# Performance work log

Measured on AMD Instinct MI355X. Metric: run time of the kernel, lower is better.

## Reference

```python
import jax, jax.numpy as jnp
import numpy as np
from jax import lax

# Model dims (mamba_ssm defaults: d_state=16, d_conv=4, expand=2, dt_rank=ceil(d_model/16))
V = 16384       # vocab_size
D = 1024        # embedding_dim / d_model
C_CLS = 128     # num_CLS_classes
D_INNER = 2 * D # expand * d_model = 2048
N = 16          # d_state
K = 4           # d_conv
DT_RANK = (D + 15) // 16  # 64
B, L = 4, 512


def setup_inputs() -> dict:
    key = jax.random.key(0)
    ks = jax.random.split(key, 12)
    s = 0.02
    tokens = jax.random.randint(ks[0], (B, L), 0, V, dtype=jnp.int64)
    embedding = jax.random.normal(ks[1], (V, D), jnp.float32) * s
    in_proj_w = jax.random.normal(ks[2], (2 * D_INNER, D), jnp.float32) * s
    conv_w = jax.random.normal(ks[3], (D_INNER, 1, K), jnp.float32) * 0.1
    conv_b = jnp.zeros((D_INNER,), jnp.float32)
    x_proj_w = jax.random.normal(ks[4], (DT_RANK + 2 * N, D_INNER), jnp.float32) * s
    dt_proj_w = jax.random.normal(ks[5], (D_INNER, DT_RANK), jnp.float32) * s
    dt_proj_b = jax.random.uniform(ks[6], (D_INNER,), jnp.float32, -4.0, -2.0)  # softplus -> small dt
    A_log = jnp.log(jnp.broadcast_to(jnp.arange(1, N + 1, dtype=jnp.float32), (D_INNER, N)))
    D_param = jnp.ones((D_INNER,), jnp.float32)
    out_proj_w = jax.random.normal(ks[7], (D, D_INNER), jnp.float32) * s
    recon_w = jax.random.normal(ks[8], (V, D), jnp.float32) * s
    cls_w = jax.random.normal(ks[9], (C_CLS, D), jnp.float32) * s
    return dict(tokens=tokens, embedding=embedding, in_proj_w=in_proj_w,
                conv_w=conv_w, conv_b=conv_b, x_proj_w=x_proj_w,
                dt_proj_w=dt_proj_w, dt_proj_b=dt_proj_b, A_log=A_log,
                D_param=D_param, out_proj_w=out_proj_w, recon_w=recon_w, cls_w=cls_w)


def _mamba(h, in_proj_w, conv_w, conv_b, x_proj_w, dt_proj_w, dt_proj_b, A_log, D_param, out_proj_w):
    # h: (B, L, D)
    xz = jnp.einsum('bld,ed->ble', h, in_proj_w)          # (B, L, 2*D_INNER)
    x, z = jnp.split(xz, 2, axis=-1)                      # each (B, L, D_INNER)
    # causal depthwise conv1d along L
    xt = jnp.swapaxes(x, 1, 2)                            # (B, D_INNER, L)
    xt = lax.conv_general_dilated(xt, conv_w, window_strides=(1,),
                                  padding=[(K - 1, 0)],
                                  feature_group_count=D_INNER,
                                  dimension_numbers=('NCH', 'OIH', 'NCH'))
    xt = xt + conv_b[None, :, None]
    x = jax.nn.silu(jnp.swapaxes(xt, 1, 2))               # (B, L, D_INNER)
    # input-dependent dt, B, C
    x_dbl = jnp.einsum('bld,ed->ble', x, x_proj_w)        # (B, L, DT_RANK+2N)
    dt, Bm, Cm = jnp.split(x_dbl, [DT_RANK, DT_RANK + N], axis=-1)
    delta = jax.nn.softplus(jnp.einsum('blr,dr->bld', dt, dt_proj_w) + dt_proj_b)  # (B,L,D_INNER)
    A = -jnp.exp(A_log)                                   # (D_INNER, N)
    dA = jnp.exp(delta[..., None] * A)                    # (B,L,D_INNER,N)
    dBx = delta[..., None] * Bm[:, :, None, :] * x[..., None]  # (B,L,D_INNER,N)
    # selective scan over time (sequential recurrence)
    dA_t = jnp.swapaxes(dA, 0, 1)                         # (L,B,D_INNER,N)
    dBx_t = jnp.swapaxes(dBx, 0, 1)
    C_t = jnp.swapaxes(Cm, 0, 1)                          # (L,B,N)
    def step(hc, inp):
        a, bx, c = inp
        hc = a * hc + bx                                  # (B,D_INNER,N)
        y = jnp.einsum('bdn,bn->bd', hc, c)
        return hc, y
    h0 = jnp.zeros((x.shape[0], D_INNER, N), x.dtype)
    _, ys = lax.scan(step, h0, (dA_t, dBx_t, C_t))
    y = jnp.swapaxes(ys, 0, 1) + x * D_param              # (B,L,D_INNER)
    y = y * jax.nn.silu(z)
    return jnp.einsum('ble,de->bld', y, out_proj_w)       # (B,L,D)


def reference(tokens, embedding, in_proj_w, conv_w, conv_b, x_proj_w,
              dt_proj_w, dt_proj_b, A_log, D_param, out_proj_w, recon_w, cls_w):
    h = embedding[tokens]                                 # (B,L,D)
    h = _mamba(h, in_proj_w, conv_w, conv_b, x_proj_w, dt_proj_w, dt_proj_b,
               A_log, D_param, out_proj_w)
    recon = jnp.einsum('bld,vd->blv', h, recon_w)         # (B,L,V)
    pooled = h.mean(axis=1)                               # mean CLS pooling assumption
    cls = jnp.einsum('bd,cd->bc', pooled, cls_w)          # (B,C_CLS)
    return (recon, cls)
```

## Files before the change

kernel.cpp:

```cpp
#include <hip/hip_runtime.h>
#include <hip/hip_bf16.h>
#include <stdint.h>

#define DIN    2048
#define MROWS  2048
#define LSEQ   512
#define NV     16384
#define DMODEL 1024
#define NC     8
#define CL     64

typedef __attribute__((ext_vector_type(8))) short bf16x8;
typedef __attribute__((ext_vector_type(4))) float f32x4;

__device__ __forceinline__ uint16_t f2bf(float f) {
  uint32_t u = __builtin_bit_cast(uint32_t, f);
  u += 0x7fffu + ((u >> 16) & 1u);
  return (uint16_t)(u >> 16);
}
__device__ __forceinline__ float bf2f(uint16_t u) {
  return __builtin_bit_cast(float, (uint32_t)u << 16);
}

__device__ __forceinline__ void gld_lds16(const uint16_t* g, uint16_t* l) {
  __builtin_amdgcn_global_load_lds(
      (const __attribute__((address_space(1))) void*)g,
      (__attribute__((address_space(3))) void*)l,
      16, 0, 0);
}

__global__ __launch_bounds__(512, 2) void gemm256_bf16_kernel(
    const uint16_t* __restrict__ A, const uint16_t* __restrict__ B,
    float* __restrict__ C, int M, int N, int K)
{
  __shared__ uint16_t lds[4 * 16384];
  const int tid = threadIdx.x;
  const int w   = tid >> 6;
  const int l   = tid & 63;

  const int nwg = gridDim.x;
  const int cpx = nwg >> 3;
  const int swz = (blockIdx.x & 7) * cpx + (blockIdx.x >> 3);
  const int nmy = M >> 8;
  const int bm  = (swz % nmy) << 8;
  const int bn  = (swz / nmy) << 8;

  const int fr = l & 15;
  const int fg = l >> 4;
  const int wr = w >> 2;
  const int wc = w & 3;

  const int srow = l >> 2;
  const int kof  = (((l & 3) ^ ((l >> 3) & 3)) << 3);
  const int ar0  = (w * 2 + 0) * 16 + srow;
  const int ar1  = (w * 2 + 1) * 16 + srow;
  const uint16_t* Ag0 = A + (size_t)(bm + ar0) * K + kof;
  const uint16_t* Ag1 = A + (size_t)(bm + ar1) * K + kof;
  const uint16_t* Bg0 = B + (size_t)(bn + ar0) * K + kof;
  const uint16_t* Bg1 = B + (size_t)(bn + ar1) * K + kof;
  const int lA0 = (w * 2 + 0) * 512;
  const int lA1 = (w * 2 + 1) * 512;
  const int lB0 = 8192 + (w * 2 + 0) * 512;
  const int lB1 = 8192 + (w * 2 + 1) * 512;

  const int axr  = ((fg ^ ((fr >> 1) & 3)) << 3);
  const int aoff = (wr * 128 + fr) * 32 + axr;
  const int boff = 8192 + (wc * 64 + fr) * 32 + axr;

  f32x4 acc[8][4] = {};
  const int NT = K >> 5;

  auto stage = [&](int t) {
    const int sb = (t & 3) << 14;
    const int k0 = t << 5;
    gld_lds16(Ag0 + k0, lds + sb + lA0);
    gld_lds16(Ag1 + k0, lds + sb + lA1);
    gld_lds16(Bg0 + k0, lds + sb + lB0);
    gld_lds16(Bg1 + k0, lds + sb + lB1);
  };
  auto compute_tile = [&](int sb) {
    bf16x8 af[8], bfr[4];
#pragma unroll
    for (int mi = 0; mi < 8; ++mi)
      af[mi] = *(const bf16x8*)(lds + sb + aoff + mi * 512);
#pragma unroll
    for (int ni = 0; ni < 4; ++ni)
      bfr[ni] = *(const bf16x8*)(lds + sb + boff + ni * 512);
    __builtin_amdgcn_s_setprio(1);
#pragma unroll
    for (int mi = 0; mi < 8; ++mi)
#pragma unroll
      for (int ni = 0; ni < 4; ++ni)
        acc[mi][ni] = __builtin_amdgcn_mfma_f32_16x16x32_bf16(af[mi], bfr[ni], acc[mi][ni], 0, 0, 0);
    __builtin_amdgcn_s_setprio(0);
  };

  stage(0); stage(1); stage(2);
  asm volatile("s_waitcnt vmcnt(8)" ::: "memory");
  __builtin_amdgcn_s_barrier();

  for (int t = 0; t < NT - 3; ++t) {
    stage(t + 3);
    compute_tile((t & 3) << 14);
    asm volatile("s_waitcnt vmcnt(8)" ::: "memory");
    __builtin_amdgcn_s_barrier();
  }
  compute_tile(((NT - 3) & 3) << 14);
  asm volatile("s_waitcnt vmcnt(4)" ::: "memory");
  __builtin_amdgcn_s_barrier();
  compute_tile(((NT - 2) & 3) << 14);
  asm volatile("s_waitcnt vmcnt(0)" ::: "memory");
  __builtin_amdgcn_s_barrier();
  compute_tile(((NT - 1) & 3) << 14);

#pragma unroll
  for (int mi = 0; mi < 8; ++mi) {
    const int r0 = bm + wr * 128 + mi * 16 + fg * 4;
#pragma unroll
    for (int ni = 0; ni < 4; ++ni) {
      const int c0 = bn + wc * 64 + ni * 16 + fr;
#pragma unroll
      for (int r = 0; r < 4; ++r)
        C[(size_t)(r0 + r) * N + c0] = acc[mi][ni][r];
    }
  }
}

__global__ __launch_bounds__(256) void gemm_bf16_kernel(
    const uint16_t* __restrict__ A, const uint16_t* __restrict__ B,
    float* __restrict__ Cf, uint16_t* __restrict__ Cbf,
    int M, int N, int K, int kchunk, const float* __restrict__ bias)
{
  __shared__ uint16_t As[128 * 32];
  __shared__ uint16_t Bs[128 * 32];
  const int tid  = threadIdx.x;
  const int wid  = tid >> 6;
  const int lane = tid & 63;
  const int bm = blockIdx.y * 128;
  const int bn = blockIdx.x * 128;
  const int k_beg = blockIdx.z * kchunk;
  float* Cout = Cf + (size_t)blockIdx.z * M * N;

  const int fr = lane & 15;
  const int fg = lane >> 4;
  const int wm = (wid >> 1) * 64;
  const int wn = (wid & 1) * 64;

  const int srow = wid * 32 + (lane >> 2);
  const int skof = (((lane & 3) ^ ((lane >> 2) & 3)) << 3);
  const uint16_t* Ag = A + (size_t)(bm + srow) * K + skof;
  const uint16_t* Bg = B + (size_t)(bn + srow) * K + skof;
  uint16_t* Al = As + wid * 1024;
  uint16_t* Bl = Bs + wid * 1024;

  const int cxr = ((fg ^ (fr & 3)) << 3);

  f32x4 acc[4][4] = {};

  for (int k0 = 0; k0 < kchunk; k0 += 32) {
    const int kk = k_beg + k0;
    gld_lds16(Ag + kk, Al);
    gld_lds16(Ag + (size_t)16 * K + kk, Al + 512);
    gld_lds16(Bg + kk, Bl);
    gld_lds16(Bg + (size_t)16 * K + kk, Bl + 512);
    asm volatile("s_waitcnt vmcnt(0)" ::: "memory");
    __syncthreads();
    bf16x8 af[4], bfr[4];
#pragma unroll
    for (int i = 0; i < 4; ++i)
      af[i] = *(const bf16x8*)(As + (wm + i * 16 + fr) * 32 + cxr);
#pragma unroll
    for (int j = 0; j < 4; ++j)
      bfr[j] = *(const bf16x8*)(Bs + (wn + j * 16 + fr) * 32 + cxr);
#pragma unroll
    for (int i = 0; i < 4; ++i)
#pragma unroll
      for (int j = 0; j < 4; ++j)
        acc[i][j] = __builtin_amdgcn_mfma_f32_16x16x32_bf16(af[i], bfr[j], acc[i][j], 0, 0, 0);
    __syncthreads();
  }

#pragma unroll
  for (int i = 0; i < 4; ++i) {
    const int r0 = bm + wm + i * 16 + fg * 4;
#pragma unroll
    for (int j = 0; j < 4; ++j) {
      const int c0 = bn + wn + j * 16 + fr;
      const float bv = bias ? bias[c0] : 0.f;
#pragma unroll
      for (int r = 0; r < 4; ++r) {
        float v = acc[i][j][r];
        if (bias) {
          const float u = v + bv;
          v = (u > 20.f) ? u : log1pf(__expf(u));
        }
        if (Cbf) Cbf[(size_t)(r0 + r) * N + c0] = f2bf(v);
        else     Cout[(size_t)(r0 + r) * N + c0] = v;
      }
    }
  }
}

__global__ __launch_bounds__(256) void cvt_weights_kernel(
    const float* __restrict__ wo, const float* __restrict__ wdt, const float* __restrict__ wx,
    uint16_t* __restrict__ wob, uint16_t* __restrict__ wdtb, uint16_t* __restrict__ wxb)
{
  const int bid = blockIdx.x;
  if (bid < 2048) {
    const int i = bid * 256 + threadIdx.x;
    const float4 v = ((const float4*)wo)[i];
    ((ushort4*)wob)[i] = make_ushort4(f2bf(v.x), f2bf(v.y), f2bf(v.z), f2bf(v.w));
  } else if (bid < 2176) {
    const int i = (bid - 2048) * 256 + threadIdx.x;
    const float4 v = ((const float4*)wdt)[i];
    ((ushort4*)wdtb)[i] = make_ushort4(f2bf(v.x), f2bf(v.y), f2bf(v.z), f2bf(v.w));
  } else {
    const int i = (bid - 2176) * 256 + threadIdx.x;
    const int r = i >> 9, c = i & 511;
    ushort4 o = make_ushort4(0, 0, 0, 0);
    if (r < 96) {
      const float4 v = ((const float4*)wx)[(size_t)r * 512 + c];
      o = make_ushort4(f2bf(v.x), f2bf(v.y), f2bf(v.z), f2bf(v.w));
    }
    ((ushort4*)wxb)[i] = o;
  }
}

__global__ __launch_bounds__(256) void reduce8_dt_kernel(
    const float* __restrict__ in, float* __restrict__ xdbl, uint16_t* __restrict__ dtb) {
  const int i = blockIdx.x * 256 + threadIdx.x;
  float s = 0.f;
#pragma unroll
  for (int z = 0; z < 8; ++z) s += in[i + (size_t)z * 262144];
  xdbl[i] = s;
  const int c = i & 127;
  if (c < 64) dtb[(i >> 7) * 64 + c] = f2bf(s);
}

__global__ __launch_bounds__(256) void reduce2_bf16_kernel(
    const float* __restrict__ in, uint16_t* __restrict__ outb, int n) {
  const int i = blockIdx.x * 256 + threadIdx.x;
  if (i >= n) return;
  outb[i] = f2bf(in[i] + in[i + (size_t)n]);
}

__global__ __launch_bounds__(256) void embed_kernel(
    const int* __restrict__ tok, const float* __restrict__ emb, uint16_t* __restrict__ out) {
  const int m = blockIdx.x;
  const int t = tok[m];
  const float4 v = ((const float4*)(emb + (size_t)t * DMODEL))[threadIdx.x];
  ((ushort4*)(out + (size_t)m * DMODEL))[threadIdx.x] =
      make_ushort4(f2bf(v.x), f2bf(v.y), f2bf(v.z), f2bf(v.w));
}

__global__ __launch_bounds__(256) void cvt_bf16_kernel(
    const float* __restrict__ in, uint16_t* __restrict__ out, int n4) {
  const int i = blockIdx.x * 256 + threadIdx.x;
  if (i >= n4) return;
  const float4 v = ((const float4*)in)[i];
  ((ushort4*)out)[i] = make_ushort4(f2bf(v.x), f2bf(v.y), f2bf(v.z), f2bf(v.w));
}

__global__ __launch_bounds__(256) void conv_silu_kernel(
    const uint16_t* __restrict__ xzb, const float* __restrict__ cw, const float* __restrict__ cb,
    uint16_t* __restrict__ xcb)
{
  const int idx = blockIdx.x * 256 + threadIdx.x;
  const int d4  = idx & 511;
  const int m   = idx >> 9;
  const int l   = m & (LSEQ - 1);
  const int d   = d4 << 2;
  const float4 cbv = *(const float4*)(cb + d);
  float a0 = cbv.x, a1 = cbv.y, a2 = cbv.z, a3 = cbv.w;
  const float4 w0 = *(const float4*)(cw + (d + 0) * 4);
  const float4 w1 = *(const float4*)(cw + (d + 1) * 4);
  const float4 w2 = *(const float4*)(cw + (d + 2) * 4);
  const float4 w3 = *(const float4*)(cw + (d + 3) * 4);
  const float wj0[4] = {w0.x, w0.y, w0.z, w0.w};
  const float wj1[4] = {w1.x, w1.y, w1.z, w1.w};
  const float wj2[4] = {w2.x, w2.y, w2.z, w2.w};
  const float wj3[4] = {w3.x, w3.y, w3.z, w3.w};
#pragma unroll
  for (int j = 0; j < 4; ++j) {
    const int lj = l - 3 + j;
    if (lj >= 0) {
      const ushort4 x = *(const ushort4*)(xzb + (size_t)(m - 3 + j) * 4096 + d);
      a0 += wj0[j] * bf2f(x.x);
      a1 += wj1[j] * bf2f(x.y);
      a2 += wj2[j] * bf2f(x.z);
      a3 += wj3[j] * bf2f(x.w);
    }
  }
  const float r0 = a0 / (1.f + __expf(-a0));
  const float r1 = a1 / (1.f + __expf(-a1));
  const float r2 = a2 / (1.f + __expf(-a2));
  const float r3 = a3 / (1.f + __expf(-a3));
  *(ushort4*)(xcb + (size_t)m * DIN + d) = make_ushort4(f2bf(r0), f2bf(r1), f2bf(r2), f2bf(r3));
}

__global__ __launch_bounds__(256) void scan_partial_kernel(
    const float* __restrict__ delta, const uint16_t* __restrict__ xcb,
    const float* __restrict__ xdbl, const float* __restrict__ A_log,
    float* __restrict__ Pb, float* __restrict__ Qb)
{
  const int q = threadIdx.x & 3;
  const int d_idx = threadIdx.x >> 2;
  const int c = blockIdx.x;
  const int d = blockIdx.y * 64 + d_idx;
  const int b = blockIdx.z;
  float Arow[4];
#pragma unroll
  for (int n = 0; n < 4; ++n)
    Arow[n] = -expf(A_log[d * 16 + q * 4 + n]);
  float P[4] = {1.f, 1.f, 1.f, 1.f};
  float Q[4] = {0.f, 0.f, 0.f, 0.f};
  const int l0 = c * CL;
#pragma unroll 4
  for (int li = 0; li < CL; ++li) {
    const int m = b * LSEQ + l0 + li;
    const float de = delta[(size_t)m * DIN + d];
    const float xv = bf2f(xcb[(size_t)m * DIN + d]);
    const float dx = de * xv;
    const float4 Bv = *(const float4*)(xdbl + (size_t)m * 128 + 64 + q * 4);
    const float bv[4] = {Bv.x, Bv.y, Bv.z, Bv.w};
#pragma unroll
    for (int n = 0; n < 4; ++n) {
      const float a = __expf(de * Arow[n]);
      P[n] *= a;
      Q[n] = a * Q[n] + dx * bv[n];
    }
  }
  const size_t o = ((size_t)(b * NC + c) * DIN + d) * 16 + q * 4;
  *(float4*)(Pb + o) = make_float4(P[0], P[1], P[2], P[3]);
  *(float4*)(Qb + o) = make_float4(Q[0], Q[1], Q[2], Q[3]);
}

__global__ __launch_bounds__(256) void scan_bounds_kernel(
    const float* __restrict__ Pb, const float* __restrict__ Qb, float* __restrict__ Hi)
{
  const int i = blockIdx.x * 256 + threadIdx.x;
  const int b = i >> 15;
  const int r = i & 32767;
  float h = 0.f;
#pragma unroll
  for (int c = 0; c < NC; ++c) {
    const size_t o = ((size_t)(b * NC + c) << 15) + r;
    Hi[o] = h;
    h = Pb[o] * h + Qb[o];
  }
}

__global__ __launch_bounds__(256) void scan_final_kernel(
    const float* __restrict__ delta, const uint16_t* __restrict__ xcb,
    const float* __restrict__ xdbl, const uint16_t* __restrict__ xzb,
    const float* __restrict__ A_log, const float* __restrict__ Dp,
    const float* __restrict__ Hi, uint16_t* __restrict__ yb)
{
  const int q = threadIdx.x & 3;
  const int d_idx = threadIdx.x >> 2;
  const int c = blockIdx.x;
  const int d = blockIdx.y * 64 + d_idx;
  const int b = blockIdx.z;
  float Arow[4];
#pragma unroll
  for (int n = 0; n < 4; ++n)
    Arow[n] = -expf(A_log[d * 16 + q * 4 + n]);
  const float dpd = Dp[d];
  const size_t o = ((size_t)(b * NC + c) * DIN + d) * 16 + q * 4;
  const float4 Hv = *(const float4*)(Hi + o);
  float h[4] = {Hv.x, Hv.y, Hv.z, Hv.w};
  const int l0 = c * CL;
#pragma unroll 2
  for (int li = 0; li < CL; ++li) {
    const int m = b * LSEQ + l0 + li;
    const float de = delta[(size_t)m * DIN + d];
    const float xv = bf2f(xcb[(size_t)m * DIN + d]);
    const float dx = de * xv;
    const float4 Bv = *(const float4*)(xdbl + (size_t)m * 128 + 64 + q * 4);
    const float4 Cv = *(const float4*)(xdbl + (size_t)m * 128 + 80 + q * 4);
    const float bv[4] = {Bv.x, Bv.y, Bv.z, Bv.w};
    const float cv[4] = {Cv.x, Cv.y, Cv.z, Cv.w};
    float yp = 0.f;
#pragma unroll
    for (int n = 0; n < 4; ++n) {
      const float a = __expf(de * Arow[n]);
      h[n] = a * h[n] + dx * bv[n];
      yp += h[n] * cv[n];
    }
    yp += __shfl_xor(yp, 1);
    yp += __shfl_xor(yp, 2);
    if (q == 0) {
      const float z = bf2f(xzb[(size_t)m * 4096 + 2048 + d]);
      const float sil = z / (1.f + __expf(-z));
      yb[(size_t)m * DIN + d] = f2bf((yp + xv * dpd) * sil);
    }
  }
}

__global__ __launch_bounds__(256) void pool1_kernel(
    const uint16_t* __restrict__ h2b, float* __restrict__ part) {
  const int b = blockIdx.x >> 4, s = blockIdx.x & 15;
  const int c = threadIdx.x * 4;
  const uint16_t* base = h2b + ((size_t)(b * LSEQ + s * 32)) * DMODEL + c;
  float a0 = 0, a1 = 0, a2 = 0, a3 = 0;
  for (int l = 0; l < 32; ++l) {
    const ushort4 v = *(const ushort4*)(base + (size_t)l * DMODEL);
    a0 += bf2f(v.x); a1 += bf2f(v.y); a2 += bf2f(v.z); a3 += bf2f(v.w);
  }
  *(float4*)(part + (size_t)blockIdx.x * DMODEL + c) = make_float4(a0, a1, a2, a3);
}

__global__ __launch_bounds__(256) void pool2_cls_kernel(
    const float* __restrict__ part, const float* __restrict__ w, float* __restrict__ out) {
  __shared__ float pl[DMODEL];
  const int b = blockIdx.x, t = threadIdx.x;
  float4 s = make_float4(0, 0, 0, 0);
  for (int k = 0; k < 16; ++k) {
    const float4 v = *(const float4*)(part + ((size_t)(b * 16 + k)) * DMODEL + t * 4);
    s.x += v.x; s.y += v.y; s.z += v.z; s.w += v.w;
  }
  const float inv = 1.f / (float)LSEQ;
  pl[t * 4 + 0] = s.x * inv; pl[t * 4 + 1] = s.y * inv;
  pl[t * 4 + 2] = s.z * inv; pl[t * 4 + 3] = s.w * inv;
  __syncthreads();
  if (t < 128) {
    const float* wr = w + (size_t)t * DMODEL;
    float acc = 0.f;
    for (int k = 0; k < DMODEL; ++k) acc += pl[k] * wr[k];
    out[b * 128 + t] = acc;
  }
}

extern "C" void kernel_launch(void* const* d_in, const int* in_sizes, int n_in,
                              void* d_out, int out_size, void* d_ws, size_t ws_size,
                              hipStream_t stream) {
  const int*   tokens    = (const int*)d_in[0];
  const float* embedding = (const float*)d_in[1];
  const float* in_proj_w = (const float*)d_in[2];
  const float* conv_w    = (const float*)d_in[3];
  const float* conv_b    = (const float*)d_in[4];
  const float* x_proj_w  = (const float*)d_in[5];
  const float* dt_proj_w = (const float*)d_in[6];
  const float* dt_proj_b = (const float*)d_in[7];
  const float* A_log     = (const float*)d_in[8];
  const float* D_param   = (const float*)d_in[9];
  const float* out_prj_w = (const float*)d_in[10];
  const float* recon_w   = (const float*)d_in[11];
  const float* cls_w     = (const float*)d_in[12];

  char* ws = (char*)d_ws;
  const size_t MB = 1024 * 1024;
  uint16_t* h_bf   = (uint16_t*)(ws + 0);
  uint16_t* w_in   = (uint16_t*)(ws + 4 * MB);
  uint16_t* xz_bf  = (uint16_t*)(ws + 12 * MB);
  uint16_t* xc_b   = (uint16_t*)(ws + 28 * MB);
  uint16_t* wx_bf  = (uint16_t*)(ws + 36 * MB);
  uint16_t* dt_bf  = (uint16_t*)(ws + 36 * MB + 512 * 1024);
  uint16_t* wdt_bf = (uint16_t*)(ws + 36 * MB + 768 * 1024);
  float*    xdbl   = (float*)(ws + 37 * MB);
  float*    delta  = (float*)(ws + 38 * MB);
  float*    Pbuf   = (float*)(ws + 54 * MB);
  float*    Qbuf   = (float*)(ws + 58 * MB);
  uint16_t* y_bf   = (uint16_t*)(ws + 62 * MB);
  uint16_t* h2_bf  = (uint16_t*)(ws + 70 * MB);
  float*    part   = (float*)(ws + 74 * MB);
  uint16_t* wout_bf = h_bf;
  float*    Hinit   = (float*)(ws + 4 * MB);
  float*    kscr    = delta;
  uint16_t* wrec_bf = (uint16_t*)(ws + 38 * MB);

  const int RECON = MROWS * NV;

  embed_kernel<<<dim3(MROWS), dim3(256), 0, stream>>>(tokens, embedding, h_bf);
  cvt_bf16_kernel<<<dim3(4096), dim3(256), 0, stream>>>(in_proj_w, w_in, 4096 * 1024 / 4);
  gemm_bf16_kernel<<<dim3(32, 16, 1), dim3(256), 0, stream>>>(h_bf, w_in, nullptr, xz_bf, MROWS, 4096, 1024, 1024, nullptr);
  cvt_weights_kernel<<<dim3(2432), dim3(256), 0, stream>>>(out_prj_w, dt_proj_w, x_proj_w, wout_bf, wdt_bf, wx_bf);
  conv_silu_kernel<<<dim3(4096), dim3(256), 0, stream>>>(xz_bf, conv_w, conv_b, xc_b);
  gemm_bf16_kernel<<<dim3(1, 16, 8), dim3(256), 0, stream>>>(xc_b, wx_bf, kscr, nullptr, MROWS, 128, 2048, 256, nullptr);
  reduce8_dt_kernel<<<dim3(1024), dim3(256), 0, stream>>>(kscr, xdbl, dt_bf);
  gemm_bf16_kernel<<<dim3(16, 16, 1), dim3(256), 0, stream>>>(dt_bf, wdt_bf, delta, nullptr, MROWS, DIN, 64, 64, dt_proj_b);
  scan_partial_kernel<<<dim3(NC, 32, 4), dim3(256), 0, stream>>>(delta, xc_b, xdbl, A_log, Pbuf, Qbuf);
  scan_bounds_kernel<<<dim3(512), dim3(256), 0, stream>>>(Pbuf, Qbuf, Hinit);
  scan_final_kernel<<<dim3(NC, 32, 4), dim3(256), 0, stream>>>(delta, xc_b, xdbl, xz_bf, A_log, D_param, Hinit, y_bf);
  gemm_bf16_kernel<<<dim3(8, 16, 2), dim3(256), 0, stream>>>(y_bf, wout_bf, kscr, nullptr, MROWS, 1024, 2048, 1024, nullptr);
  reduce2_bf16_kernel<<<dim3(8192), dim3(256), 0, stream>>>(kscr, h2_bf, MROWS * 1024);
  cvt_bf16_kernel<<<dim3(16384), dim3(256), 0, stream>>>(recon_w, wrec_bf, NV * 1024 / 4);
  gemm256_bf16_kernel<<<dim3(512), dim3(512), 0, stream>>>(h2_bf, wrec_bf, (float*)d_out, MROWS, NV, 1024);
  pool1_kernel<<<dim3(64), dim3(256), 0, stream>>>(h2_bf, part);
  pool2_cls_kernel<<<dim3(4), dim3(256), 0, stream>>>(part, cls_w, (float*)d_out + RECON);
}
```

Baseline: 359.2 us.

## Fuse scan stages, merge conversion kernels, store delta in bf16, drop split-K

Merges the embedding gather and all weight conversions into one kernel. Fuses the three chunked-scan kernels into one block-level kernel that does the chunk carry in shared memory. Stores delta as bf16 instead of fp32, and runs the out_proj GEMM without split-K so it writes bf16 directly, which removes the reduce2 kernel. This cuts launches and HBM round trips for the P/Q/H buffers and delta. In exchange the out_proj GEMM runs fewer blocks over a longer K, and delta loses precision.

```diff
diff --git a/kernel.cpp b/kernel.cpp
--- a/kernel.cpp
+++ b/kernel.cpp
@@ -201,21 +201,35 @@
   }
 }
 
-__global__ __launch_bounds__(256) void cvt_weights_kernel(
-    const float* __restrict__ wo, const float* __restrict__ wdt, const float* __restrict__ wx,
-    uint16_t* __restrict__ wob, uint16_t* __restrict__ wdtb, uint16_t* __restrict__ wxb)
+__global__ __launch_bounds__(256) void mega_cvt_kernel(
+    const int* __restrict__ tok, const float* __restrict__ emb,
+    const float* __restrict__ wi, const float* __restrict__ wo,
+    const float* __restrict__ wdt, const float* __restrict__ wx,
+    uint16_t* __restrict__ hb, uint16_t* __restrict__ wib,
+    uint16_t* __restrict__ wob, uint16_t* __restrict__ wdtb,
+    uint16_t* __restrict__ wxb)
 {
   const int bid = blockIdx.x;
   if (bid < 2048) {
-    const int i = bid * 256 + threadIdx.x;
+    const int m = bid;
+    const int t = tok[m];
+    const float4 v = ((const float4*)(emb + (size_t)t * DMODEL))[threadIdx.x];
+    ((ushort4*)(hb + (size_t)m * DMODEL))[threadIdx.x] =
+        make_ushort4(f2bf(v.x), f2bf(v.y), f2bf(v.z), f2bf(v.w));
+  } else if (bid < 6144) {
+    const int i = (bid - 2048) * 256 + threadIdx.x;
+    const float4 v = ((const float4*)wi)[i];
+    ((ushort4*)wib)[i] = make_ushort4(f2bf(v.x), f2bf(v.y), f2bf(v.z), f2bf(v.w));
+  } else if (bid < 8192) {
+    const int i = (bid - 6144) * 256 + threadIdx.x;
     const float4 v = ((const float4*)wo)[i];
     ((ushort4*)wob)[i] = make_ushort4(f2bf(v.x), f2bf(v.y), f2bf(v.z), f2bf(v.w));
-  } else if (bid < 2176) {
-    const int i = (bid - 2048) * 256 + threadIdx.x;
+  } else if (bid < 8320) {
+    const int i = (bid - 8192) * 256 + threadIdx.x;
     const float4 v = ((const float4*)wdt)[i];
     ((ushort4*)wdtb)[i] = make_ushort4(f2bf(v.x), f2bf(v.y), f2bf(v.z), f2bf(v.w));
   } else {
-    const int i = (bid - 2176) * 256 + threadIdx.x;
+    const int i = (bid - 8320) * 256 + threadIdx.x;
     const int r = i >> 9, c = i & 511;
     ushort4 o = make_ushort4(0, 0, 0, 0);
     if (r < 96) {
@@ -235,22 +249,6 @@
   xdbl[i] = s;
   const int c = i & 127;
   if (c < 64) dtb[(i >> 7) * 64 + c] = f2bf(s);
-}
-
-__global__ __launch_bounds__(256) void reduce2_bf16_kernel(
-    const float* __restrict__ in, uint16_t* __restrict__ outb, int n) {
-  const int i = blockIdx.x * 256 + threadIdx.x;
-  if (i >= n) return;
-  outb[i] = f2bf(in[i] + in[i + (size_t)n]);
-}
-
-__global__ __launch_bounds__(256) void embed_kernel(
-    const int* __restrict__ tok, const float* __restrict__ emb, uint16_t* __restrict__ out) {
-  const int m = blockIdx.x;
-  const int t = tok[m];
-  const float4 v = ((const float4*)(emb + (size_t)t * DMODEL))[threadIdx.x];
-  ((ushort4*)(out + (size_t)m * DMODEL))[threadIdx.x] =
-      make_ushort4(f2bf(v.x), f2bf(v.y), f2bf(v.z), f2bf(v.w));
 }
 
 __global__ __launch_bounds__(256) void cvt_bf16_kernel(
@@ -298,27 +296,32 @@
   *(ushort4*)(xcb + (size_t)m * DIN + d) = make_ushort4(f2bf(r0), f2bf(r1), f2bf(r2), f2bf(r3));
 }
 
-__global__ __launch_bounds__(256) void scan_partial_kernel(
-    const float* __restrict__ delta, const uint16_t* __restrict__ xcb,
-    const float* __restrict__ xdbl, const float* __restrict__ A_log,
-    float* __restrict__ Pb, float* __restrict__ Qb)
+__global__ __launch_bounds__(256) void scan_fused_kernel(
+    const uint16_t* __restrict__ delta_bf, const uint16_t* __restrict__ xcb,
+    const float* __restrict__ xdbl, const uint16_t* __restrict__ xzb,
+    const float* __restrict__ A_log, const float* __restrict__ Dp,
+    uint16_t* __restrict__ yb)
 {
+  __shared__ float Ps[NC][8][4][4];
+  __shared__ float Qs[NC][8][4][4];
+  __shared__ float Hs[NC][8][4][4];
   const int q = threadIdx.x & 3;
-  const int d_idx = threadIdx.x >> 2;
-  const int c = blockIdx.x;
-  const int d = blockIdx.y * 64 + d_idx;
-  const int b = blockIdx.z;
+  const int d_idx = (threadIdx.x >> 2) & 7;
+  const int c = threadIdx.x >> 5;
+  const int d = blockIdx.x * 8 + d_idx;
+  const int b = blockIdx.y;
   float Arow[4];
 #pragma unroll
   for (int n = 0; n < 4; ++n)
     Arow[n] = -expf(A_log[d * 16 + q * 4 + n]);
+  const int l0 = c * CL;
+
   float P[4] = {1.f, 1.f, 1.f, 1.f};
   float Q[4] = {0.f, 0.f, 0.f, 0.f};
-  const int l0 = c * CL;
 #pragma unroll 4
   for (int li = 0; li < CL; ++li) {
     const int m = b * LSEQ + l0 + li;
-    const float de = delta[(size_t)m * DIN + d];
+    const float de = bf2f(delta_bf[(size_t)m * DIN + d]);
     const float xv = bf2f(xcb[(size_t)m * DIN + d]);
     const float dx = de * xv;
     const float4 Bv = *(const float4*)(xdbl + (size_t)m * 128 + 64 + q * 4);
@@ -330,50 +333,34 @@
       Q[n] = a * Q[n] + dx * bv[n];
     }
   }
-  const size_t o = ((size_t)(b * NC + c) * DIN + d) * 16 + q * 4;
-  *(float4*)(Pb + o) = make_float4(P[0], P[1], P[2], P[3]);
-  *(float4*)(Qb + o) = make_float4(Q[0], Q[1], Q[2], Q[3]);
-}
-
-__global__ __launch_bounds__(256) void scan_bounds_kernel(
-    const float* __restrict__ Pb, const float* __restrict__ Qb, float* __restrict__ Hi)
-{
-  const int i = blockIdx.x * 256 + threadIdx.x;
-  const int b = i >> 15;
-  const int r = i & 32767;
-  float h = 0.f;
-#pragma unroll
-  for (int c = 0; c < NC; ++c) {
-    const size_t o = ((size_t)(b * NC + c) << 15) + r;
-    Hi[o] = h;
-    h = Pb[o] * h + Qb[o];
-  }
-}
-
-__global__ __launch_bounds__(256) void scan_final_kernel(
-    const float* __restrict__ delta, const uint16_t* __restrict__ xcb,
-    const float* __restrict__ xdbl, const uint16_t* __restrict__ xzb,
-    const float* __restrict__ A_log, const float* __restrict__ Dp,
-    const float* __restrict__ Hi, uint16_t* __restrict__ yb)
-{
-  const int q = threadIdx.x & 3;
-  const int d_idx = threadIdx.x >> 2;
-  const int c = blockIdx.x;
-  const int d = blockIdx.y * 64 + d_idx;
-  const int b = blockIdx.z;
-  float Arow[4];
-#pragma unroll
-  for (int n = 0; n < 4; ++n)
-    Arow[n] = -expf(A_log[d * 16 + q * 4 + n]);
+#pragma unroll
+  for (int n = 0; n < 4; ++n) {
+    Ps[c][d_idx][q][n] = P[n];
+    Qs[c][d_idx][q][n] = Q[n];
+  }
+  __syncthreads();
+
+  if (threadIdx.x < 32) {
+    float h[4] = {0.f, 0.f, 0.f, 0.f};
+#pragma unroll
+    for (int cc = 0; cc < NC; ++cc) {
+#pragma unroll
+      for (int n = 0; n < 4; ++n) {
+        Hs[cc][d_idx][q][n] = h[n];
+        h[n] = Ps[cc][d_idx][q][n] * h[n] + Qs[cc][d_idx][q][n];
+      }
+    }
+  }
+  __syncthreads();
+
+  float h[4];
+#pragma unroll
+  for (int n = 0; n < 4; ++n) h[n] = Hs[c][d_idx][q][n];
   const float dpd = Dp[d];
-  const size_t o = ((size_t)(b * NC + c) * DIN + d) * 16 + q * 4;
-  const float4 Hv = *(const float4*)(Hi + o);
-  float h[4] = {Hv.x, Hv.y, Hv.z, Hv.w};
-  const int l0 = c * CL;
 #pragma unroll 2
   for (int li = 0; li < CL; ++li) {
     const int m = b * LSEQ + l0 + li;
-    const float de = delta[(size_t)m * DIN + d];
+    const float de = bf2f(delta_bf[(size_t)m * DIN + d]);
     const float xv = bf2f(xcb[(size_t)m * DIN + d]);
     const float dx = de * xv;
     const float4 Bv = *(const float4*)(xdbl + (size_t)m * 128 + 64 + q * 4);
@@ -458,32 +445,26 @@
   uint16_t* dt_bf  = (uint16_t*)(ws + 36 * MB + 512 * 1024);
   uint16_t* wdt_bf = (uint16_t*)(ws + 36 * MB + 768 * 1024);
   float*    xdbl   = (float*)(ws + 37 * MB);
-  float*    delta  = (float*)(ws + 38 * MB);
-  float*    Pbuf   = (float*)(ws + 54 * MB);
-  float*    Qbuf   = (float*)(ws + 58 * MB);
-  uint16_t* y_bf   = (uint16_t*)(ws + 62 * MB);
-  uint16_t* h2_bf  = (uint16_t*)(ws + 70 * MB);
-  float*    part   = (float*)(ws + 74 * MB);
-  uint16_t* wout_bf = h_bf;
-  float*    Hinit   = (float*)(ws + 4 * MB);
-  float*    kscr    = delta;
-  uint16_t* wrec_bf = (uint16_t*)(ws + 38 * MB);
+  uint16_t* delt_b = (uint16_t*)(ws + 38 * MB);
+  float*    kscr   = (float*)(ws + 46 * MB);
+  uint16_t* y_bf   = (uint16_t*)(ws + 54 * MB);
+  uint16_t* h2_bf  = (uint16_t*)(ws + 62 * MB);
+  uint16_t* wout_bf= (uint16_t*)(ws + 66 * MB);
+  float*    part   = (float*)(ws + 70 * MB);
+  uint16_t* wrec_bf= (uint16_t*)(ws + 71 * MB);
 
   const int RECON = MROWS * NV;
 
-  embed_kernel<<<dim3(MROWS), dim3(256), 0, stream>>>(tokens, embedding, h_bf);
-  cvt_bf16_kernel<<<dim3(4096), dim3(256), 0, stream>>>(in_proj_w, w_in, 4096 * 1024 / 4);
+  mega_cvt_kernel<<<dim3(8576), dim3(256), 0, stream>>>(
+      tokens, embedding, in_proj_w, out_prj_w, dt_proj_w, x_proj_w,
+      h_bf, w_in, wout_bf, wdt_bf, wx_bf);
   gemm_bf16_kernel<<<dim3(32, 16, 1), dim3(256), 0, stream>>>(h_bf, w_in, nullptr, xz_bf, MROWS, 4096, 1024, 1024, nullptr);
-  cvt_weights_kernel<<<dim3(2432), dim3(256), 0, stream>>>(out_prj_w, dt_proj_w, x_proj_w, wout_bf, wdt_bf, wx_bf);
   conv_silu_kernel<<<dim3(4096), dim3(256), 0, stream>>>(xz_bf, conv_w, conv_b, xc_b);
   gemm_bf16_kernel<<<dim3(1, 16, 8), dim3(256), 0, stream>>>(xc_b, wx_bf, kscr, nullptr, MROWS, 128, 2048, 256, nullptr);
   reduce8_dt_kernel<<<dim3(1024), dim3(256), 0, stream>>>(kscr, xdbl, dt_bf);
-  gemm_bf16_kernel<<<dim3(16, 16, 1), dim3(256), 0, stream>>>(dt_bf, wdt_bf, delta, nullptr, MROWS, DIN, 64, 64, dt_proj_b);
-  scan_partial_kernel<<<dim3(NC, 32, 4), dim3(256), 0, stream>>>(delta, xc_b, xdbl, A_log, Pbuf, Qbuf);
-  scan_bounds_kernel<<<dim3(512), dim3(256), 0, stream>>>(Pbuf, Qbuf, Hinit);
-  scan_final_kernel<<<dim3(NC, 32, 4), dim3(256), 0, stream>>>(delta, xc_b, xdbl, xz_bf, A_log, D_param, Hinit, y_bf);
-  gemm_bf16_kernel<<<dim3(8, 16, 2), dim3(256), 0, stream>>>(y_bf, wout_bf, kscr, nullptr, MROWS, 1024, 2048, 1024, nullptr);
-  reduce2_bf16_kernel<<<dim3(8192), dim3(256), 0, stream>>>(kscr, h2_bf, MROWS * 1024);
+  gemm_bf16_kernel<<<dim3(16, 16, 1), dim3(256), 0, stream>>>(dt_bf, wdt_bf, nullptr, delt_b, MROWS, DIN, 64, 64, dt_proj_b);
+  scan_fused_kernel<<<dim3(DIN / 8, 4), dim3(256), 0, stream>>>(delt_b, xc_b, xdbl, xz_bf, A_log, D_param, y_bf);
+  gemm_bf16_kernel<<<dim3(8, 16, 1), dim3(256), 0, stream>>>(y_bf, wout_bf, nullptr, h2_bf, MROWS, 1024, 2048, 2048, nullptr);
   cvt_bf16_kernel<<<dim3(16384), dim3(256), 0, stream>>>(recon_w, wrec_bf, NV * 1024 / 4);
   gemm256_bf16_kernel<<<dim3(512), dim3(512), 0, stream>>>(h2_bf, wrec_bf, (float*)d_out, MROWS, NV, 1024);
   pool1_kernel<<<dim3(64), dim3(256), 0, stream>>>(h2_bf, part);
```

After: 402.5 us, median of 4. +12.1%, slower.
